# Optimization experiments

Hardware: AMD Instinct MI355X
Metric: run time of the kernel (lower is better)

The kernel has to match this reference:

```python
import jax, jax.numpy as jnp
import numpy as np

B, N, F, FOBS, D = 4, 1024, 128, 32, 128
K_HOP = 3  # os.environ k_hop default 3


def setup_inputs() -> dict:
    key = jax.random.key(0)
    k0, k1, k2, k3, k4 = jax.random.split(key, 5)
    X = jax.random.normal(k0, (B, N, F), jnp.float32)
    # xavier-ish scales for params
    a_link = jax.random.normal(k1, (FOBS, 1), jnp.float32) * (1.414 / np.sqrt(FOBS + 1))
    W0 = jax.random.normal(k2, (F, D), jnp.float32) * np.sqrt(2.0 / (F + D))
    W1 = jax.random.normal(k3, (D, D), jnp.float32) * np.sqrt(1.0 / D)
    W2 = jax.random.normal(k4, (D, D), jnp.float32) * np.sqrt(1.0 / D)
    return {"X": X, "a_link": a_link, "W0": W0, "W1": W1, "W2": W2}


def reference(X, a_link, W0, W1, W2):
    eye = jnp.eye(N, dtype=X.dtype)

    def per_graph(Xb):  # Xb: [N, F]
        h = Xb[:, :FOBS]                                   # [N, FOBS]
        # e_ij = a_link^T |h_i - h_j|
        e = jnp.einsum('ijf,fo->ij', jnp.abs(h[:, None, :] - h[None, :, :]), a_link)
        A = jax.nn.sigmoid(e)
        A = A * (1.0 - eye)                                # zero diagonal (A - diag(diag(A)))
        Dm = jnp.zeros_like(A)                             # diag(diag(A)) is zero after removal
        A_hat = A + eye
        d_inv_sqrt = jnp.sum(A_hat, axis=1) ** -0.5        # row sums (dim=1 in mini_batch path)
        norm = d_inv_sqrt[:, None] * A_hat * d_inv_sqrt[None, :]  # D^-1/2 A_hat D^-1/2
        H = norm @ (Xb @ W0)                               # k = 0
        for Wk in (W1, W2):                                # k = 1 .. K_HOP-1 (norm detached in torch)
            H = jax.lax.stop_gradient(norm) @ (H @ Wk)
        return jax.nn.relu(H), A, Dm

    Hs, As, Ds = jax.vmap(per_graph)(X)
    return Hs, As, X, Ds
```

## Files before the change

### kernel.cpp

```cpp
#include <hip/hip_runtime.h>
#include <math.h>

#define BB 4
#define NN 1024
#define FF 128
#define DD 128
#define FOBS 32

typedef __attribute__((ext_vector_type(8))) short bfrag;
typedef __attribute__((ext_vector_type(4))) float ffrag;
typedef __attribute__((ext_vector_type(4))) unsigned short us4;

__device__ __forceinline__ unsigned short f2bf(float x) {
    unsigned u = __builtin_bit_cast(unsigned, x);
    u += 0x7fffu + ((u >> 16) & 1u);
    return (unsigned short)(u >> 16);
}
__device__ __forceinline__ float bf2f(unsigned short s) {
    unsigned u = (unsigned)s << 16;
    return __builtin_bit_cast(float, u);
}
__device__ __forceinline__ void gload16(const void* g, void* l) {
    __builtin_amdgcn_global_load_lds((const __attribute__((address_space(1))) unsigned*)g,
                                     (__attribute__((address_space(3))) unsigned*)l, 16, 0, 0);
}
__device__ __forceinline__ void compute_dinv16(const float* __restrict__ Pp, int b, int n0,
                                               int tid, float* dinv_s) {
    int r = tid >> 4, p = tid & 15;
    float s = Pp[((size_t)b * NN + n0 + r) * 16 + p];
    s += __shfl_xor(s, 1);
    s += __shfl_xor(s, 2);
    s += __shfl_xor(s, 4);
    s += __shfl_xor(s, 8);
    if (p == 0) dinv_s[r] = rsqrtf(1.f + s);
}

__global__ __launch_bounds__(256) void zero_f4(float4* __restrict__ p, int n4) {
    int i = blockIdx.x * 256 + threadIdx.x;
    if (i < n4) p[i] = make_float4(0.f, 0.f, 0.f, 0.f);
}

__global__ __launch_bounds__(256) void adj_kernel(const float* __restrict__ X,
                                                  const float* __restrict__ a_link,
                                                  const float* __restrict__ W0,
                                                  const float* __restrict__ W1,
                                                  const float* __restrict__ W2,
                                                  float* __restrict__ A,
                                                  unsigned short* __restrict__ Abf,
                                                  unsigned short* __restrict__ Xbf,
                                                  unsigned short* __restrict__ Wt,
                                                  float* __restrict__ Pp,
                                                  float* __restrict__ Xo,
                                                  float* __restrict__ Zd) {
    int tid = threadIdx.x;
    if (blockIdx.z == 5) {
        if (Zd) {
            int q = blockIdx.y * 16 + blockIdx.x;
            float4* Z = (float4*)Zd;
#pragma unroll
            for (int p = 0; p < 16; p++)
                Z[(size_t)q * 4096 + p * 256 + tid] = make_float4(0.f, 0.f, 0.f, 0.f);
        }
        return;
    }
    if (blockIdx.z == 4) {
        int q = (blockIdx.y * 16 + blockIdx.x) * 256 + tid;
        if (q < 49152) {
            int m = q >> 14, rem = q & 16383, fp = rem >> 7, f = rem & 127;
            const float* W = (m == 0) ? W0 : (m == 1) ? W1 : W2;
            Wt[q] = f2bf(W[(size_t)f * 128 + fp]);
        } else {
            int u = q - 49152;
#pragma unroll
            for (int p = 0; p < 8; p++) {
                size_t i4 = (size_t)u + (size_t)p * 16384;
                float4 v = *(const float4*)&X[i4 * 4];
                us4 o; o[0] = f2bf(v.x); o[1] = f2bf(v.y); o[2] = f2bf(v.z); o[3] = f2bf(v.w);
                *(us4*)&Xbf[i4 * 4] = o;
            }
        }
        return;
    }
    int b = blockIdx.z, i0 = blockIdx.y * 64, j0 = blockIdx.x * 64;
    __shared__ float hi[64][FOBS + 1];
    __shared__ float hj[64][FOBS + 1];
    __shared__ float av[FOBS];
    __shared__ float part_s[64][16];
    const float* Xb = X + (size_t)b * NN * FF;
    if (j0 == 0) {
#pragma unroll
        for (int p = 0; p < 8; p++) {
            int c = p * 256 + tid, r = c >> 5, qq = c & 31;
            *(float4*)&Xo[((size_t)b * NN + i0 + r) * FF + qq * 4] =
                *(const float4*)&Xb[(size_t)(i0 + r) * FF + qq * 4];
        }
    }
#pragma unroll
    for (int l = 0; l < 8; l++) {
        int idx = l * 256 + tid;
        int r = idx >> 5, f = idx & 31;
        hi[r][f] = Xb[(size_t)(i0 + r) * FF + f];
        hj[r][f] = Xb[(size_t)(j0 + r) * FF + f];
    }
    if (tid < FOBS) av[tid] = a_link[tid];
    __syncthreads();

    int ty = tid >> 4, tx = tid & 15;
    int ir = ty * 4, jc = tx * 4;
    float acc[4][4] = {};
#pragma unroll
    for (int f = 0; f < FOBS; f++) {
        float a = av[f];
        float x[4], y[4];
#pragma unroll
        for (int r = 0; r < 4; r++) x[r] = hi[ir + r][f];
#pragma unroll
        for (int c = 0; c < 4; c++) y[c] = hj[jc + c][f];
#pragma unroll
        for (int r = 0; r < 4; r++)
#pragma unroll
            for (int c = 0; c < 4; c++)
                acc[r][c] += fabsf(x[r] - y[c]) * a;
    }
    float* Ab = A + (size_t)b * NN * NN;
    unsigned short* Abb = Abf + (size_t)b * NN * NN;
#pragma unroll
    for (int r = 0; r < 4; r++) {
        int gi = i0 + ir + r;
        float vv[4];
        float rs = 0.f;
#pragma unroll
        for (int c = 0; c < 4; c++) {
            int gj = j0 + jc + c;
            float sg = 1.f / (1.f + __expf(-acc[r][c]));
            vv[c] = (gi == gj) ? 0.f : sg;
            rs += vv[c];
        }
        *(float4*)&Ab[(size_t)gi * NN + (j0 + jc)] = make_float4(vv[0], vv[1], vv[2], vv[3]);
        us4 o; o[0] = f2bf(vv[0]); o[1] = f2bf(vv[1]); o[2] = f2bf(vv[2]); o[3] = f2bf(vv[3]);
        *(us4*)&Abb[(size_t)gi * NN + (j0 + jc)] = o;
        part_s[ir + r][tx] = rs;
    }
    __syncthreads();
    if (tid < 64) {
        float s = 0.f;
#pragma unroll
        for (int k = 0; k < 16; k++) s += part_s[tid][k];
        Pp[((size_t)b * NN + i0 + tid) * 16 + blockIdx.x] = s;
    }
}

__global__ __launch_bounds__(256) void gw0_kernel(const unsigned short* __restrict__ Xbf,
                                                  const unsigned short* __restrict__ Wt0,
                                                  const float* __restrict__ Pp,
                                                  unsigned short* __restrict__ TtOut) {
    int b = blockIdx.y;
    int n0 = blockIdx.x * 16;
    __shared__ unsigned short Wt_s[128 * 128];
    __shared__ unsigned short H_s[16 * 128];
    __shared__ float dinv_s[16];
    int tid = threadIdx.x;
    compute_dinv16(Pp, b, n0, tid, dinv_s);
    const unsigned short* Hb = Xbf + (size_t)b * NN * DD;
#pragma unroll
    for (int p = 0; p < 8; p++) {
        int c = p * 256 + tid, row = c >> 4, kc = c & 15;
        gload16(Wt0 + (size_t)row * 128 + ((kc ^ (row & 7)) * 8), Wt_s + (size_t)c * 8);
    }
    {
        int c = tid, row = c >> 4, kc = c & 15;
        gload16(Hb + (size_t)(n0 + row) * 128 + ((kc ^ (row & 7)) * 8), H_s + (size_t)c * 8);
    }
    __syncthreads();

    int w = tid >> 6, l = tid & 63, lr = l & 15, lg = l >> 4;
    ffrag acc[2] = {};
#pragma unroll
    for (int ks = 0; ks < 4; ks++) {
        int k0 = ks * 32 + lg * 8;
        bfrag a[2], bb;
#pragma unroll
        for (int rb = 0; rb < 2; rb++) {
            int row = w * 32 + rb * 16 + lr;
            int byt = (row * 256 + k0 * 2) ^ ((row & 7) << 4);
            a[rb] = *(const bfrag*)((const char*)Wt_s + byt);
        }
        {
            int row = lr;
            int byt = (row * 256 + k0 * 2) ^ ((row & 7) << 4);
            bb = *(const bfrag*)((const char*)H_s + byt);
        }
#pragma unroll
        for (int rb = 0; rb < 2; rb++)
            acc[rb] = __builtin_amdgcn_mfma_f32_16x16x32_bf16(a[rb], bb, acc[rb], 0, 0, 0);
    }
    unsigned short* Ttb = TtOut + (size_t)b * DD * NN;
    int nl = lr;
    float dv = dinv_s[nl];
#pragma unroll
    for (int rb = 0; rb < 2; rb++)
#pragma unroll
        for (int r = 0; r < 4; r++) {
            int f = w * 32 + rb * 16 + lg * 4 + r;
            Ttb[(size_t)f * NN + n0 + nl] = f2bf(acc[rb][r] * dv);
        }
}

template <int MODE>
__global__ __launch_bounds__(256) void ga_kernel(const unsigned short* __restrict__ Abf,
                                                 const unsigned short* __restrict__ Tt,
                                                 const unsigned short* __restrict__ WtN,
                                                 const float* __restrict__ Pp,
                                                 unsigned short* __restrict__ TtN,
                                                 float* __restrict__ HsF) {
    int b = blockIdx.y, n0 = blockIdx.x * 16;
    __shared__ unsigned short T_s[3 * 128 * 64];
    __shared__ unsigned short A_s[3 * 16 * 64];
    __shared__ unsigned short W_s[MODE == 0 ? 128 * 128 : 64];
    __shared__ float dinv_s[16];
    int tid = threadIdx.x;
    const unsigned short* Ttb = Tt + (size_t)b * DD * NN;
    const unsigned short* Ab = Abf + (size_t)b * NN * NN;

    compute_dinv16(Pp, b, n0, tid, dinv_s);

    if (MODE == 0) {
#pragma unroll
        for (int p = 0; p < 8; p++) {
            int c = p * 256 + tid, row = c >> 4, kc = c & 15;
            gload16(WtN + (size_t)row * 128 + ((kc ^ (row & 7)) * 8), W_s + (size_t)c * 8);
        }
    }
    auto stageT = [&](int buf, int kt) {
#pragma unroll
        for (int p = 0; p < 4; p++) {
            int c = p * 256 + tid, row = c >> 3, kc = c & 7;
            gload16(Ttb + (size_t)row * NN + kt + ((kc ^ (row & 7)) * 8),
                    T_s + (size_t)buf * (128 * 64) + (size_t)c * 8);
        }
        int c = tid & 127, row = c >> 3, kc = c & 7;
        gload16(Ab + (size_t)(n0 + row) * NN + kt + ((kc ^ (row & 7)) * 8),
                A_s + (size_t)buf * (16 * 64) + (size_t)c * 8);
    };
    stageT(0, 0);
    stageT(1, 64);

    int w = tid >> 6, l = tid & 63, lr = l & 15, lg = l >> 4;
    ffrag acc[2] = {};
    int cur = 0, sb = 2;
    for (int t = 0; t < 16; t++) {
        if (t <= 13) stageT(sb, (t + 2) * 64);
        if (t < 14)       asm volatile("s_waitcnt vmcnt(10)" ::: "memory");
        else if (t == 14) asm volatile("s_waitcnt vmcnt(5)"  ::: "memory");
        else              asm volatile("s_waitcnt vmcnt(0)"  ::: "memory");
        __builtin_amdgcn_s_barrier();
        asm volatile("" ::: "memory");
        const unsigned short* Tc = T_s + (size_t)cur * (128 * 64);
        const unsigned short* Ac = A_s + (size_t)cur * (16 * 64);
#pragma unroll
        for (int ks = 0; ks < 2; ks++) {
            int k0 = ks * 32 + lg * 8;
            bfrag a[2], bb;
#pragma unroll
            for (int rb = 0; rb < 2; rb++) {
                int row = w * 32 + rb * 16 + lr;
                int byt = (row * 128 + k0 * 2) ^ ((row & 7) << 4);
                a[rb] = *(const bfrag*)((const char*)Tc + byt);
            }
            {
                int row = lr;
                int byt = (row * 128 + k0 * 2) ^ ((row & 7) << 4);
                bb = *(const bfrag*)((const char*)Ac + byt);
            }
#pragma unroll
            for (int rb = 0; rb < 2; rb++)
                acc[rb] = __builtin_amdgcn_mfma_f32_16x16x32_bf16(a[rb], bb, acc[rb], 0, 0, 0);
        }
        asm volatile("s_waitcnt lgkmcnt(0)" ::: "memory");
        __builtin_amdgcn_s_barrier();
        cur = (cur == 2) ? 0 : cur + 1;
        sb = (sb == 2) ? 0 : sb + 1;
    }

    int nl = lr;
    float dv = dinv_s[nl];
    if (MODE == 1) {
#pragma unroll
        for (int rb = 0; rb < 2; rb++) {
            int f0 = w * 32 + rb * 16 + lg * 4;
            float v[4];
#pragma unroll
            for (int r = 0; r < 4; r++) {
                float idv = bf2f(Ttb[(size_t)(f0 + r) * NN + n0 + nl]);
                v[r] = fmaxf((acc[rb][r] + idv) * dv, 0.f);
            }
            *(float4*)&HsF[((size_t)b * NN + n0 + nl) * DD + f0] = make_float4(v[0], v[1], v[2], v[3]);
        }
        return;
    }
    unsigned short* H_s = T_s;
#pragma unroll
    for (int rb = 0; rb < 2; rb++) {
        int f0 = w * 32 + rb * 16 + lg * 4;
        us4 o;
#pragma unroll
        for (int r = 0; r < 4; r++) {
            float idv = bf2f(Ttb[(size_t)(f0 + r) * NN + n0 + nl]);
            o[r] = f2bf((acc[rb][r] + idv) * dv);
        }
        int byt = (nl * 256 + f0 * 2) ^ ((nl & 7) << 4);
        *(us4*)((char*)H_s + byt) = o;
    }
    __syncthreads();
    ffrag acc2[2] = {};
#pragma unroll
    for (int ks = 0; ks < 4; ks++) {
        int k0 = ks * 32 + lg * 8;
        bfrag a2[2], b2;
#pragma unroll
        for (int rb = 0; rb < 2; rb++) {
            int row = w * 32 + rb * 16 + lr;
            int byt = (row * 256 + k0 * 2) ^ ((row & 7) << 4);
            a2[rb] = *(const bfrag*)((const char*)W_s + byt);
        }
        {
            int row = lr;
            int byt = (row * 256 + k0 * 2) ^ ((row & 7) << 4);
            b2 = *(const bfrag*)((const char*)H_s + byt);
        }
#pragma unroll
        for (int rb = 0; rb < 2; rb++)
            acc2[rb] = __builtin_amdgcn_mfma_f32_16x16x32_bf16(a2[rb], b2, acc2[rb], 0, 0, 0);
    }
    unsigned short* TtNb = TtN + (size_t)b * DD * NN;
#pragma unroll
    for (int rb = 0; rb < 2; rb++)
#pragma unroll
        for (int r = 0; r < 4; r++) {
            int f2 = w * 32 + rb * 16 + lg * 4 + r;
            TtNb[(size_t)f2 * NN + n0 + nl] = f2bf(acc2[rb][r] * dv);
        }
}

extern "C" void kernel_launch(void* const* d_in, const int* in_sizes, int n_in,
                              void* d_out, int out_size, void* d_ws, size_t ws_size,
                              hipStream_t stream) {
    const float* X      = (const float*)d_in[0];
    const float* a_link = (const float*)d_in[1];
    const float* W0     = (const float*)d_in[2];
    const float* W1     = (const float*)d_in[3];
    const float* W2     = (const float*)d_in[4];
    float* out = (float*)d_out;

    const size_t HND = (size_t)BB * NN * DD;
    const size_t HNN = (size_t)BB * NN * NN;
    float* Hs = out;
    float* As = out + HND;
    float* Xo = out + HND + HNN;
    float* Ds = out + 2 * HND + HNN;

    const size_t NEED = 11894784;
    bool usews = (ws_size >= NEED);
    char* scr = usews ? (char*)d_ws : (char*)Ds;

    unsigned short* Abf = (unsigned short*)(scr);
    unsigned short* Xbf = (unsigned short*)(scr + 8388608);
    unsigned short* TtA = (unsigned short*)(scr + 9437184);
    unsigned short* TtB = (unsigned short*)(scr + 10485760);
    unsigned short* Wt  = (unsigned short*)(scr + 11534336);
    float* Pp           = (float*)(scr + 11632640);

    adj_kernel<<<dim3(16, 16, usews ? 6 : 5), 256, 0, stream>>>(
        X, a_link, W0, W1, W2, As, Abf, Xbf, Wt, Pp, Xo, usews ? Ds : nullptr);

    gw0_kernel<<<dim3(64, BB), 256, 0, stream>>>(Xbf, Wt, Pp, TtA);
    ga_kernel<0><<<dim3(64, BB), 256, 0, stream>>>(Abf, TtA, Wt + 16384, Pp, TtB, nullptr);
    ga_kernel<0><<<dim3(64, BB), 256, 0, stream>>>(Abf, TtB, Wt + 32768, Pp, TtA, nullptr);
    ga_kernel<1><<<dim3(64, BB), 256, 0, stream>>>(Abf, TtA, nullptr, Pp, nullptr, Hs);

    if (!usews)
        zero_f4<<<dim3(4096), 256, 0, stream>>>((float4*)Ds, (int)(HNN / 4));
}
```

Measured before the change: 48.70 us.

## Reassociate GCN hops: precompute X·W0·W1·W2, build normalized bf16 adjacency per block

Uses associativity (norm@X@W0@W1@W2 chain) to fold all weight multiplications into a single upfront transform: W0·W1 is precomputed in the adj kernel, and t0_kernel computes X·W01·W2 once, so each propagation kernel becomes a pure norm@T product. The bf16 adjacency copy is dropped; instead each ga block reads its fp32 A rows, applies D^-1/2(A+I)D^-1/2 into shared memory as bf16, and streams only T tiles. This removes the 8 MB bf16 adjacency write and the per-hop weight GEMMs, at the cost of reading fp32 A (twice the bytes) three times and a serial 128-length dot loop per thread for W0·W1.

```diff
diff --git a/kernel.cpp b/kernel.cpp
--- a/kernel.cpp
+++ b/kernel.cpp
@@ -16,23 +16,9 @@
     u += 0x7fffu + ((u >> 16) & 1u);
     return (unsigned short)(u >> 16);
 }
-__device__ __forceinline__ float bf2f(unsigned short s) {
-    unsigned u = (unsigned)s << 16;
-    return __builtin_bit_cast(float, u);
-}
 __device__ __forceinline__ void gload16(const void* g, void* l) {
     __builtin_amdgcn_global_load_lds((const __attribute__((address_space(1))) unsigned*)g,
                                      (__attribute__((address_space(3))) unsigned*)l, 16, 0, 0);
-}
-__device__ __forceinline__ void compute_dinv16(const float* __restrict__ Pp, int b, int n0,
-                                               int tid, float* dinv_s) {
-    int r = tid >> 4, p = tid & 15;
-    float s = Pp[((size_t)b * NN + n0 + r) * 16 + p];
-    s += __shfl_xor(s, 1);
-    s += __shfl_xor(s, 2);
-    s += __shfl_xor(s, 4);
-    s += __shfl_xor(s, 8);
-    if (p == 0) dinv_s[r] = rsqrtf(1.f + s);
 }
 
 __global__ __launch_bounds__(256) void zero_f4(float4* __restrict__ p, int n4) {
@@ -45,10 +31,10 @@
                                                   const float* __restrict__ W0,
                                                   const float* __restrict__ W1,
                                                   const float* __restrict__ W2,
-                                                  float* __restrict__ A,
-                                                  unsigned short* __restrict__ Abf,
+                                                  float* __restrict__ As,
                                                   unsigned short* __restrict__ Xbf,
-                                                  unsigned short* __restrict__ Wt,
+                                                  unsigned short* __restrict__ W01t,
+                                                  unsigned short* __restrict__ W2t,
                                                   float* __restrict__ Pp,
                                                   float* __restrict__ Xo,
                                                   float* __restrict__ Zd) {
@@ -65,15 +51,20 @@
     }
     if (blockIdx.z == 4) {
         int q = (blockIdx.y * 16 + blockIdx.x) * 256 + tid;
-        if (q < 49152) {
-            int m = q >> 14, rem = q & 16383, fp = rem >> 7, f = rem & 127;
-            const float* W = (m == 0) ? W0 : (m == 1) ? W1 : W2;
-            Wt[q] = f2bf(W[(size_t)f * 128 + fp]);
+        if (q < 16384) {
+            int g = q >> 7, f = q & 127;
+            float s = 0.f;
+            for (int h = 0; h < 128; h++) s += W0[f * 128 + h] * W1[h * 128 + g];
+            W01t[q] = f2bf(s);
+        } else if (q < 32768) {
+            int e = q - 16384;
+            int f2 = e >> 7, g = e & 127;
+            W2t[e] = f2bf(W2[g * 128 + f2]);
         } else {
-            int u = q - 49152;
-#pragma unroll
-            for (int p = 0; p < 8; p++) {
-                size_t i4 = (size_t)u + (size_t)p * 16384;
+            int u = q - 32768;
+#pragma unroll
+            for (int p = 0; p < 4; p++) {
+                size_t i4 = (size_t)u + (size_t)p * 32768;
                 float4 v = *(const float4*)&X[i4 * 4];
                 us4 o; o[0] = f2bf(v.x); o[1] = f2bf(v.y); o[2] = f2bf(v.z); o[3] = f2bf(v.w);
                 *(us4*)&Xbf[i4 * 4] = o;
@@ -122,13 +113,11 @@
             for (int c = 0; c < 4; c++)
                 acc[r][c] += fabsf(x[r] - y[c]) * a;
     }
-    float* Ab = A + (size_t)b * NN * NN;
-    unsigned short* Abb = Abf + (size_t)b * NN * NN;
+    float* Ab = As + (size_t)b * NN * NN;
 #pragma unroll
     for (int r = 0; r < 4; r++) {
         int gi = i0 + ir + r;
-        float vv[4];
-        float rs = 0.f;
+        float vv[4]; float rs = 0.f;
 #pragma unroll
         for (int c = 0; c < 4; c++) {
             int gj = j0 + jc + c;
@@ -137,8 +126,6 @@
             rs += vv[c];
         }
         *(float4*)&Ab[(size_t)gi * NN + (j0 + jc)] = make_float4(vv[0], vv[1], vv[2], vv[3]);
-        us4 o; o[0] = f2bf(vv[0]); o[1] = f2bf(vv[1]); o[2] = f2bf(vv[2]); o[3] = f2bf(vv[3]);
-        *(us4*)&Abb[(size_t)gi * NN + (j0 + jc)] = o;
         part_s[ir + r][tx] = rs;
     }
     __syncthreads();
@@ -150,31 +137,47 @@
     }
 }
 
-__global__ __launch_bounds__(256) void gw0_kernel(const unsigned short* __restrict__ Xbf,
-                                                  const unsigned short* __restrict__ Wt0,
-                                                  const float* __restrict__ Pp,
-                                                  unsigned short* __restrict__ TtOut) {
-    int b = blockIdx.y;
-    int n0 = blockIdx.x * 16;
-    __shared__ unsigned short Wt_s[128 * 128];
-    __shared__ unsigned short H_s[16 * 128];
-    __shared__ float dinv_s[16];
+__global__ __launch_bounds__(256) void t0_kernel(const unsigned short* __restrict__ Xbf,
+                                                 const unsigned short* __restrict__ W01t,
+                                                 const unsigned short* __restrict__ W2t,
+                                                 const float* __restrict__ Pp,
+                                                 unsigned short* __restrict__ TtX,
+                                                 float* __restrict__ dinvG) {
+    int bid = blockIdx.x;
+    int b = bid >> 6, n0 = (bid & 63) * 16;
+    __shared__ unsigned short W01s[128 * 128];
+    __shared__ unsigned short W2s[128 * 128];
+    __shared__ unsigned short Xps[16 * 128];
+    __shared__ unsigned short Ps[16 * 128];
     int tid = threadIdx.x;
-    compute_dinv16(Pp, b, n0, tid, dinv_s);
-    const unsigned short* Hb = Xbf + (size_t)b * NN * DD;
+    const unsigned short* Xb = Xbf + (size_t)b * NN * DD;
 #pragma unroll
     for (int p = 0; p < 8; p++) {
         int c = p * 256 + tid, row = c >> 4, kc = c & 15;
-        gload16(Wt0 + (size_t)row * 128 + ((kc ^ (row & 7)) * 8), Wt_s + (size_t)c * 8);
+        gload16(W01t + (size_t)row * 128 + ((kc ^ (row & 7)) * 8), W01s + (size_t)c * 8);
+    }
+#pragma unroll
+    for (int p = 0; p < 8; p++) {
+        int c = p * 256 + tid, row = c >> 4, kc = c & 15;
+        gload16(W2t + (size_t)row * 128 + ((kc ^ (row & 7)) * 8), W2s + (size_t)c * 8);
     }
     {
         int c = tid, row = c >> 4, kc = c & 15;
-        gload16(Hb + (size_t)(n0 + row) * 128 + ((kc ^ (row & 7)) * 8), H_s + (size_t)c * 8);
+        gload16(Xb + (size_t)(n0 + row) * 128 + ((kc ^ (row & 7)) * 8), Xps + (size_t)c * 8);
+    }
+    {
+        int r = tid >> 4, p = tid & 15;
+        float s = Pp[((size_t)b * NN + n0 + r) * 16 + p];
+        s += __shfl_xor(s, 1);
+        s += __shfl_xor(s, 2);
+        s += __shfl_xor(s, 4);
+        s += __shfl_xor(s, 8);
+        if (p == 0) dinvG[(size_t)b * NN + n0 + r] = rsqrtf(1.f + s);
     }
     __syncthreads();
 
     int w = tid >> 6, l = tid & 63, lr = l & 15, lg = l >> 4;
-    ffrag acc[2] = {};
+    ffrag pacc[2] = {};
 #pragma unroll
     for (int ks = 0; ks < 4; ks++) {
         int k0 = ks * 32 + lg * 8;
@@ -183,83 +186,118 @@
         for (int rb = 0; rb < 2; rb++) {
             int row = w * 32 + rb * 16 + lr;
             int byt = (row * 256 + k0 * 2) ^ ((row & 7) << 4);
-            a[rb] = *(const bfrag*)((const char*)Wt_s + byt);
+            a[rb] = *(const bfrag*)((const char*)W01s + byt);
         }
         {
-            int row = lr;
+            int byt = (lr * 256 + k0 * 2) ^ ((lr & 7) << 4);
+            bb = *(const bfrag*)((const char*)Xps + byt);
+        }
+#pragma unroll
+        for (int rb = 0; rb < 2; rb++)
+            pacc[rb] = __builtin_amdgcn_mfma_f32_16x16x32_bf16(a[rb], bb, pacc[rb], 0, 0, 0);
+    }
+#pragma unroll
+    for (int rb = 0; rb < 2; rb++) {
+        int g0 = w * 32 + rb * 16 + lg * 4;
+        us4 o;
+#pragma unroll
+        for (int r = 0; r < 4; r++) o[r] = f2bf(pacc[rb][r]);
+        int byt = (lr * 256 + g0 * 2) ^ ((lr & 7) << 4);
+        *(us4*)((char*)Ps + byt) = o;
+    }
+    __syncthreads();
+    ffrag tacc[2] = {};
+#pragma unroll
+    for (int ks = 0; ks < 4; ks++) {
+        int k0 = ks * 32 + lg * 8;
+        bfrag a2[2], b2;
+#pragma unroll
+        for (int rb = 0; rb < 2; rb++) {
+            int row = w * 32 + rb * 16 + lr;
             int byt = (row * 256 + k0 * 2) ^ ((row & 7) << 4);
-            bb = *(const bfrag*)((const char*)H_s + byt);
+            a2[rb] = *(const bfrag*)((const char*)W2s + byt);
+        }
+        {
+            int byt = (lr * 256 + k0 * 2) ^ ((lr & 7) << 4);
+            b2 = *(const bfrag*)((const char*)Ps + byt);
         }
 #pragma unroll
         for (int rb = 0; rb < 2; rb++)
-            acc[rb] = __builtin_amdgcn_mfma_f32_16x16x32_bf16(a[rb], bb, acc[rb], 0, 0, 0);
-    }
-    unsigned short* Ttb = TtOut + (size_t)b * DD * NN;
-    int nl = lr;
-    float dv = dinv_s[nl];
+            tacc[rb] = __builtin_amdgcn_mfma_f32_16x16x32_bf16(a2[rb], b2, tacc[rb], 0, 0, 0);
+    }
+    unsigned short* Tb = TtX + (size_t)b * DD * NN;
 #pragma unroll
     for (int rb = 0; rb < 2; rb++)
 #pragma unroll
         for (int r = 0; r < 4; r++) {
-            int f = w * 32 + rb * 16 + lg * 4 + r;
-            Ttb[(size_t)f * NN + n0 + nl] = f2bf(acc[rb][r] * dv);
-        }
-}
-
-template <int MODE>
-__global__ __launch_bounds__(256) void ga_kernel(const unsigned short* __restrict__ Abf,
-                                                 const unsigned short* __restrict__ Tt,
-                                                 const unsigned short* __restrict__ WtN,
-                                                 const float* __restrict__ Pp,
-                                                 unsigned short* __restrict__ TtN,
+            int f2 = w * 32 + rb * 16 + lg * 4 + r;
+            Tb[(size_t)f2 * NN + n0 + lr] = f2bf(tacc[rb][r]);
+        }
+}
+
+template <int LAST>
+__global__ __launch_bounds__(256) void ga_kernel(const float* __restrict__ As,
+                                                 const float* __restrict__ dinvG,
+                                                 const unsigned short* __restrict__ Tin,
+                                                 unsigned short* __restrict__ Tout,
                                                  float* __restrict__ HsF) {
-    int b = blockIdx.y, n0 = blockIdx.x * 16;
+    int bid = blockIdx.x;
+    int b = bid >> 6, n0 = (bid & 63) * 16;
     __shared__ unsigned short T_s[3 * 128 * 64];
-    __shared__ unsigned short A_s[3 * 16 * 64];
-    __shared__ unsigned short W_s[MODE == 0 ? 128 * 128 : 64];
-    __shared__ float dinv_s[16];
+    __shared__ unsigned short S_s[16 * 1024];
+    __shared__ float dinvF[NN];
     int tid = threadIdx.x;
-    const unsigned short* Ttb = Tt + (size_t)b * DD * NN;
-    const unsigned short* Ab = Abf + (size_t)b * NN * NN;
-
-    compute_dinv16(Pp, b, n0, tid, dinv_s);
-
-    if (MODE == 0) {
-#pragma unroll
-        for (int p = 0; p < 8; p++) {
-            int c = p * 256 + tid, row = c >> 4, kc = c & 15;
-            gload16(WtN + (size_t)row * 128 + ((kc ^ (row & 7)) * 8), W_s + (size_t)c * 8);
-        }
-    }
+    const unsigned short* Tb = Tin + (size_t)b * DD * NN;
+
     auto stageT = [&](int buf, int kt) {
 #pragma unroll
         for (int p = 0; p < 4; p++) {
             int c = p * 256 + tid, row = c >> 3, kc = c & 7;
-            gload16(Ttb + (size_t)row * NN + kt + ((kc ^ (row & 7)) * 8),
+            gload16(Tb + (size_t)row * NN + kt + ((kc ^ (row & 7)) * 8),
                     T_s + (size_t)buf * (128 * 64) + (size_t)c * 8);
         }
-        int c = tid & 127, row = c >> 3, kc = c & 7;
-        gload16(Ab + (size_t)(n0 + row) * NN + kt + ((kc ^ (row & 7)) * 8),
-                A_s + (size_t)buf * (16 * 64) + (size_t)c * 8);
     };
     stageT(0, 0);
     stageT(1, 64);
+
+    {
+        *(float4*)&dinvF[tid * 4] = *(const float4*)&dinvG[(size_t)b * NN + tid * 4];
+    }
+    __syncthreads();
+    {
+        int row = tid >> 4, gi = n0 + row;
+        const float* Ar = As + ((size_t)b * NN + gi) * NN;
+        float di = dinvF[gi];
+#pragma unroll
+        for (int cc = 0; cc < 16; cc++) {
+            int col = (tid & 15) * 4 + cc * 64;
+            float4 a4 = *(const float4*)&Ar[col];
+            us4 o;
+            o[0] = f2bf(di * dinvF[col + 0] * (a4.x + ((col + 0) == gi ? 1.f : 0.f)));
+            o[1] = f2bf(di * dinvF[col + 1] * (a4.y + ((col + 1) == gi ? 1.f : 0.f)));
+            o[2] = f2bf(di * dinvF[col + 2] * (a4.z + ((col + 2) == gi ? 1.f : 0.f)));
+            o[3] = f2bf(di * dinvF[col + 3] * (a4.w + ((col + 3) == gi ? 1.f : 0.f)));
+            int byt = (row * 2048 + col * 2) ^ ((row & 7) << 4);
+            *(us4*)((char*)S_s + byt) = o;
+        }
+    }
+    __syncthreads();
 
     int w = tid >> 6, l = tid & 63, lr = l & 15, lg = l >> 4;
     ffrag acc[2] = {};
     int cur = 0, sb = 2;
     for (int t = 0; t < 16; t++) {
         if (t <= 13) stageT(sb, (t + 2) * 64);
-        if (t < 14)       asm volatile("s_waitcnt vmcnt(10)" ::: "memory");
-        else if (t == 14) asm volatile("s_waitcnt vmcnt(5)"  ::: "memory");
-        else              asm volatile("s_waitcnt vmcnt(0)"  ::: "memory");
+        if (t < 14)       asm volatile("s_waitcnt vmcnt(8)" ::: "memory");
+        else if (t == 14) asm volatile("s_waitcnt vmcnt(4)" ::: "memory");
+        else              asm volatile("s_waitcnt vmcnt(0)" ::: "memory");
         __builtin_amdgcn_s_barrier();
         asm volatile("" ::: "memory");
         const unsigned short* Tc = T_s + (size_t)cur * (128 * 64);
-        const unsigned short* Ac = A_s + (size_t)cur * (16 * 64);
 #pragma unroll
         for (int ks = 0; ks < 2; ks++) {
             int k0 = ks * 32 + lg * 8;
+            int kg = t * 64 + k0;
             bfrag a[2], bb;
 #pragma unroll
             for (int rb = 0; rb < 2; rb++) {
@@ -268,9 +306,8 @@
                 a[rb] = *(const bfrag*)((const char*)Tc + byt);
             }
             {
-                int row = lr;
-                int byt = (row * 128 + k0 * 2) ^ ((row & 7) << 4);
-                bb = *(const bfrag*)((const char*)Ac + byt);
+                int byt = (lr * 2048 + kg * 2) ^ ((lr & 7) << 4);
+                bb = *(const bfrag*)((const char*)S_s + byt);
             }
 #pragma unroll
             for (int rb = 0; rb < 2; rb++)
@@ -282,64 +319,25 @@
         sb = (sb == 2) ? 0 : sb + 1;
     }
 
-    int nl = lr;
-    float dv = dinv_s[nl];
-    if (MODE == 1) {
+    if (LAST) {
 #pragma unroll
         for (int rb = 0; rb < 2; rb++) {
             int f0 = w * 32 + rb * 16 + lg * 4;
             float v[4];
 #pragma unroll
+            for (int r = 0; r < 4; r++) v[r] = fmaxf(acc[rb][r], 0.f);
+            *(float4*)&HsF[((size_t)b * NN + n0 + lr) * DD + f0] = make_float4(v[0], v[1], v[2], v[3]);
+        }
+    } else {
+        unsigned short* Ob = Tout + (size_t)b * DD * NN;
+#pragma unroll
+        for (int rb = 0; rb < 2; rb++)
+#pragma unroll
             for (int r = 0; r < 4; r++) {
-                float idv = bf2f(Ttb[(size_t)(f0 + r) * NN + n0 + nl]);
-                v[r] = fmaxf((acc[rb][r] + idv) * dv, 0.f);
+                int f = w * 32 + rb * 16 + lg * 4 + r;
+                Ob[(size_t)f * NN + n0 + lr] = f2bf(acc[rb][r]);
             }
-            *(float4*)&HsF[((size_t)b * NN + n0 + nl) * DD + f0] = make_float4(v[0], v[1], v[2], v[3]);
-        }
-        return;
-    }
-    unsigned short* H_s = T_s;
-#pragma unroll
-    for (int rb = 0; rb < 2; rb++) {
-        int f0 = w * 32 + rb * 16 + lg * 4;
-        us4 o;
-#pragma unroll
-        for (int r = 0; r < 4; r++) {
-            float idv = bf2f(Ttb[(size_t)(f0 + r) * NN + n0 + nl]);
-            o[r] = f2bf((acc[rb][r] + idv) * dv);
-        }
-        int byt = (nl * 256 + f0 * 2) ^ ((nl & 7) << 4);
-        *(us4*)((char*)H_s + byt) = o;
-    }
-    __syncthreads();
-    ffrag acc2[2] = {};
-#pragma unroll
-    for (int ks = 0; ks < 4; ks++) {
-        int k0 = ks * 32 + lg * 8;
-        bfrag a2[2], b2;
-#pragma unroll
-        for (int rb = 0; rb < 2; rb++) {
-            int row = w * 32 + rb * 16 + lr;
-            int byt = (row * 256 + k0 * 2) ^ ((row & 7) << 4);
-            a2[rb] = *(const bfrag*)((const char*)W_s + byt);
-        }
-        {
-            int row = lr;
-            int byt = (row * 256 + k0 * 2) ^ ((row & 7) << 4);
-            b2 = *(const bfrag*)((const char*)H_s + byt);
-        }
-#pragma unroll
-        for (int rb = 0; rb < 2; rb++)
-            acc2[rb] = __builtin_amdgcn_mfma_f32_16x16x32_bf16(a2[rb], b2, acc2[rb], 0, 0, 0);
-    }
-    unsigned short* TtNb = TtN + (size_t)b * DD * NN;
-#pragma unroll
-    for (int rb = 0; rb < 2; rb++)
-#pragma unroll
-        for (int r = 0; r < 4; r++) {
-            int f2 = w * 32 + rb * 16 + lg * 4 + r;
-            TtNb[(size_t)f2 * NN + n0 + nl] = f2bf(acc2[rb][r] * dv);
-        }
+    }
 }
 
 extern "C" void kernel_launch(void* const* d_in, const int* in_sizes, int n_in,
@@ -359,24 +357,24 @@
     float* Xo = out + HND + HNN;
     float* Ds = out + 2 * HND + HNN;
 
-    const size_t NEED = 11894784;
+    const size_t NEED = 3489792;
     bool usews = (ws_size >= NEED);
     char* scr = usews ? (char*)d_ws : (char*)Ds;
 
-    unsigned short* Abf = (unsigned short*)(scr);
-    unsigned short* Xbf = (unsigned short*)(scr + 8388608);
-    unsigned short* TtA = (unsigned short*)(scr + 9437184);
-    unsigned short* TtB = (unsigned short*)(scr + 10485760);
-    unsigned short* Wt  = (unsigned short*)(scr + 11534336);
-    float* Pp           = (float*)(scr + 11632640);
+    unsigned short* Xbf  = (unsigned short*)(scr);
+    unsigned short* TtX  = (unsigned short*)(scr + 1048576);
+    unsigned short* TtY  = (unsigned short*)(scr + 2097152);
+    unsigned short* W01t = (unsigned short*)(scr + 3145728);
+    unsigned short* W2t  = (unsigned short*)(scr + 3178496);
+    float* Pp            = (float*)(scr + 3211264);
+    float* dinvG         = (float*)(scr + 3473408);
 
     adj_kernel<<<dim3(16, 16, usews ? 6 : 5), 256, 0, stream>>>(
-        X, a_link, W0, W1, W2, As, Abf, Xbf, Wt, Pp, Xo, usews ? Ds : nullptr);
-
-    gw0_kernel<<<dim3(64, BB), 256, 0, stream>>>(Xbf, Wt, Pp, TtA);
-    ga_kernel<0><<<dim3(64, BB), 256, 0, stream>>>(Abf, TtA, Wt + 16384, Pp, TtB, nullptr);
-    ga_kernel<0><<<dim3(64, BB), 256, 0, stream>>>(Abf, TtB, Wt + 32768, Pp, TtA, nullptr);
-    ga_kernel<1><<<dim3(64, BB), 256, 0, stream>>>(Abf, TtA, nullptr, Pp, nullptr, Hs);
+        X, a_link, W0, W1, W2, As, Xbf, W01t, W2t, Pp, Xo, usews ? Ds : nullptr);
+    t0_kernel<<<dim3(256), 256, 0, stream>>>(Xbf, W01t, W2t, Pp, TtX, dinvG);
+    ga_kernel<0><<<dim3(256), 256, 0, stream>>>(As, dinvG, TtX, TtY, nullptr);
+    ga_kernel<0><<<dim3(256), 256, 0, stream>>>(As, dinvG, TtY, TtX, nullptr);
+    ga_kernel<1><<<dim3(256), 256, 0, stream>>>(As, dinvG, TtX, nullptr, Hs);
 
     if (!usews)
         zero_f4<<<dim3(4096), 256, 0, stream>>>((float4*)Ds, (int)(HNN / 4));
```

Measured after the change: 56.66 us. 16.3% more time.
